# Performance work log

Measured on AMD Instinct MI355X. Metric: run time of the kernel, lower is better.

Reference implementation:

```python
import jax, jax.numpy as jnp
import numpy as np

N = 50000   # nodes
E = 800000  # edges (avg degree 16)
D = 128     # input feature dim
H = 128     # hidden dim
C = 10      # num classes
G = 16      # graphs in batch


def setup_inputs() -> dict:
    key = jax.random.key(0)
    ks = jax.random.split(key, 12)
    def w(k, shape):
        return jax.random.normal(k, shape, jnp.float32) / np.sqrt(shape[0]).astype(np.float32)
    return {
        "h": jax.random.normal(ks[0], (N, D), jnp.float32),
        "src": jax.random.randint(ks[1], (E,), 0, N, jnp.int32),
        "dst": jax.random.randint(ks[2], (E,), 0, N, jnp.int32),
        "graph_ids": jnp.sort(jax.random.randint(ks[3], (N,), 0, G, jnp.int32)),
        "W1a": w(ks[4], (D, H)), "b1a": jnp.zeros((H,), jnp.float32),
        "W2a": w(ks[5], (H, H)), "b2a": jnp.zeros((H,), jnp.float32),
        "W1b": w(ks[6], (H, H)), "b1b": jnp.zeros((H,), jnp.float32),
        "W2b": w(ks[7], (H, H)), "b2b": jnp.zeros((H,), jnp.float32),
        "Wc1": w(ks[8], (H, H)), "bc1": jnp.zeros((H,), jnp.float32),
        "Wc2": w(ks[9], (H, C)), "bc2": jnp.zeros((C,), jnp.float32),
    }


def _gin_layer(h, src, dst, W1, b1, W2, b2):
    # GIN aggregation, eps=0: z_i = h_i + sum_{j in N(i)} h_j
    agg = jax.ops.segment_sum(h[src], dst, num_segments=N)
    z = h + agg
    # 2-layer MLP apply function with relu activation ('relu' arg of GINLayer)
    z = jax.nn.relu(z @ W1 + b1)
    return jax.nn.relu(z @ W2 + b2)


def reference(h, src, dst, graph_ids, W1a, b1a, W2a, b2a,
              W1b, b1b, W2b, b2b, Wc1, bc1, Wc2, bc2):
    h = _gin_layer(h, src, dst, W1a, b1a, W2a, b2a)   # [N, H]
    h = _gin_layer(h, src, dst, W1b, b1b, W2b, b2b)   # [N, H]
    # dgl.mean_nodes over the batched graph
    sums = jax.ops.segment_sum(h, graph_ids, num_segments=G)                # [G, H]
    cnts = jax.ops.segment_sum(jnp.ones((N, 1), h.dtype), graph_ids, num_segments=G)
    h_g = sums / jnp.maximum(cnts, 1.0)
    # cls MLP: linear -> relu -> linear (logits)
    out = jax.nn.relu(h_g @ Wc1 + bc1) @ Wc2 + bc2    # [G, C]
    return out
```

## Files before the change

kernel.cpp:

```cpp
#include <hip/hip_runtime.h>
#include <stdint.h>

#define NN 50000
#define EE 800000
#define DD 128
#define GG 16
#define CC 10
#define NBK 196
#define BCH 4096
#define SMAX 5120
#define FT (NBK * NBK)
#define NSCN ((FT + 255) / 256)
#define NT 782

typedef unsigned short u16;
typedef __bf16 bf16x8 __attribute__((ext_vector_type(8)));
typedef float f32x4 __attribute__((ext_vector_type(4)));
typedef unsigned int u32x4 __attribute__((ext_vector_type(4)));
typedef float fl4 __attribute__((ext_vector_type(4)));

__device__ inline u16 f2bf(float f) {
    unsigned u = __float_as_uint(f);
    u = u + 0x7fffu + ((u >> 16) & 1u);
    return (u16)(u >> 16);
}
__device__ inline unsigned pack2(float a, float b) {
    return (unsigned)f2bf(a) | ((unsigned)f2bf(b) << 16);
}
__device__ inline float bf2f(unsigned bits16) { return __uint_as_float(bits16 << 16); }
__device__ inline void acc8(float* a, uint4 v) {
    a[0] += __uint_as_float(v.x << 16); a[1] += __uint_as_float(v.x & 0xffff0000u);
    a[2] += __uint_as_float(v.y << 16); a[3] += __uint_as_float(v.y & 0xffff0000u);
    a[4] += __uint_as_float(v.z << 16); a[5] += __uint_as_float(v.z & 0xffff0000u);
    a[6] += __uint_as_float(v.w << 16); a[7] += __uint_as_float(v.w & 0xffff0000u);
}
__device__ inline void mand(uint4& v, int p) {
    unsigned m = p ? 0xffffffffu : 0u;
    v.x &= m; v.y &= m; v.z &= m; v.w &= m;
}
__device__ inline void nt_store16(void* p, uint4 v) {
    u32x4 x; x.x = v.x; x.y = v.y; x.z = v.z; x.w = v.w;
    __builtin_nontemporal_store(x, (u32x4*)p);
}
__device__ inline float4 nt_loadf4(const float* p) {
    fl4 x = __builtin_nontemporal_load((const fl4*)p);
    float4 r; r.x = x.x; r.y = x.y; r.z = x.z; r.w = x.w;
    return r;
}

#define PZ (GG * DD)
#define PC (NN * DD / 4)
#define PW (4 * DD * DD)
#define PTOT (PZ + PC + PW)
#define PBLK ((PTOT + 255) / 256)

__global__ __launch_bounds__(256) void prepsort_kernel(
    const float* __restrict__ h,
    const float* __restrict__ a, const float* __restrict__ b,
    const float* __restrict__ c, const float* __restrict__ d,
    int* __restrict__ zbase, u16* __restrict__ H0, u16* __restrict__ wt,
    const int* __restrict__ dst, int* __restrict__ counts) {
    __shared__ int hist[NBK];
    int blk = blockIdx.x, t = threadIdx.x;
    if (blk < NBK) {
        for (int i = t; i < NBK; i += 256) hist[i] = 0;
        __syncthreads();
        int e0 = blk * BCH, e1 = min(e0 + BCH, EE);
        for (int e = e0 + t; e < e1; e += 256) atomicAdd(&hist[dst[e] >> 8], 1);
        __syncthreads();
        for (int i = t; i < NBK; i += 256) counts[i * NBK + blk] = hist[i];
        return;
    }
    int i = (blk - NBK) * 256 + t;
    if (i < PZ) { zbase[i] = 0; return; }
    i -= PZ;
    if (i < PC) {
        int j = i * 4;
        float4 v = nt_loadf4(h + j);
        ushort4 o;
        o.x = f2bf(v.x); o.y = f2bf(v.y); o.z = f2bf(v.z); o.w = f2bf(v.w);
        *(ushort4*)(H0 + j) = o;
        return;
    }
    i -= PC;
    if (i < PW) {
        int m = i >> 14, r = i & 16383, k = r >> 7, j = r & 127;
        const float* W = (m == 0) ? a : (m == 1) ? b : (m == 2) ? c : d;
        wt[(m << 14) + (j << 7) + k] = f2bf(W[(k << 7) + j]);
    }
}

__global__ __launch_bounds__(256) void scanA_kernel(int* __restrict__ counts,
                                                    int* __restrict__ bsum) {
    __shared__ int tmp[256];
    int t = threadIdx.x, idx = blockIdx.x * 256 + t;
    int v = (idx < FT) ? counts[idx] : 0;
    tmp[t] = v; __syncthreads();
    for (int off = 1; off < 256; off <<= 1) {
        int x = (t >= off) ? tmp[t - off] : 0;
        __syncthreads();
        tmp[t] += x;
        __syncthreads();
    }
    if (idx < FT) counts[idx] = tmp[t] - v;
    if (t == 255) bsum[blockIdx.x] = tmp[255];
}

__global__ __launch_bounds__(256) void scanB_kernel(int* __restrict__ bsum,
                                                    const int* __restrict__ gids,
                                                    int* __restrict__ gstart) {
    __shared__ int tmp[256];
    int t = threadIdx.x;
    if (t <= GG) {
        int lo = 0, hi = NN;
        while (lo < hi) { int mid = (lo + hi) >> 1; if (gids[mid] < t) lo = mid + 1; else hi = mid; }
        gstart[t] = lo;
    }
    int v = (t < NSCN) ? bsum[t] : 0;
    tmp[t] = v; __syncthreads();
    for (int off = 1; off < 256; off <<= 1) {
        int x = (t >= off) ? tmp[t - off] : 0;
        __syncthreads();
        tmp[t] += x;
        __syncthreads();
    }
    if (t < NSCN) bsum[t] = tmp[t] - v;
}

__global__ __launch_bounds__(256) void scanC_kernel(int* __restrict__ counts,
                                                    const int* __restrict__ bsum) {
    int idx = blockIdx.x * 256 + threadIdx.x;
    if (idx < FT) counts[idx] += bsum[blockIdx.x];
}

__global__ __launch_bounds__(256) void sortP3_kernel(const int* __restrict__ src,
                                                     const int* __restrict__ dst,
                                                     const int* __restrict__ counts,
                                                     int* __restrict__ epack) {
    __shared__ int lhist[NBK + 1];
    __shared__ int lcur[NBK];
    __shared__ int goff[NBK];
    __shared__ int tmp[256];
    __shared__ int sbuf[BCH];
    int b = blockIdx.x, t = threadIdx.x;
    int e0 = b * BCH, e1 = min(e0 + BCH, EE), n = e1 - e0;

    for (int i = t; i < NBK; i += 256) lhist[i] = 0;
    __syncthreads();
    for (int e = e0 + t; e < e1; e += 256) atomicAdd(&lhist[dst[e] >> 8], 1);
    __syncthreads();
    int v = (t < NBK) ? lhist[t] : 0;
    tmp[t] = v; __syncthreads();
    for (int off = 1; off < 256; off <<= 1) {
        int x = (t >= off) ? tmp[t - off] : 0;
        __syncthreads();
        tmp[t] += x;
        __syncthreads();
    }
    if (t < NBK) {
        int excl = tmp[t] - v;
        lcur[t] = excl;
        lhist[t] = excl;
        goff[t] = counts[t * NBK + b] - excl;
    }
    if (t == 0) lhist[NBK] = n;
    __syncthreads();
    for (int e = e0 + t; e < e1; e += 256) {
        int dd = dst[e], s = src[e];
        int p = atomicAdd(&lcur[dd >> 8], 1);
        sbuf[p] = (s << 8) | (dd & 255);
    }
    __syncthreads();
    for (int i = t; i < n; i += 256) {
        int pk = sbuf[i];
        int lo = 0, hi = NBK - 1;
        while (lo < hi) { int mid = (lo + hi + 1) >> 1; if (lhist[mid] <= i) lo = mid; else hi = mid - 1; }
        epack[goff[lo] + i] = pk;
    }
}

__global__ __launch_bounds__(256) void sortP4_kernel(const int* __restrict__ epack,
                                                     const int* __restrict__ counts,
                                                     int* __restrict__ offs,
                                                     int* __restrict__ ssrc) {
    __shared__ int hist[256];
    __shared__ int curs[256];
    __shared__ int stage[SMAX];
    int j = blockIdx.x, t = threadIdx.x;
    int n0 = j << 8;
    int b0 = counts[j * NBK];
    int b1 = (j < NBK - 1) ? counts[(j + 1) * NBK] : EE;
    hist[t] = 0;
    __syncthreads();
    for (int e = b0 + t; e < b1; e += 256) atomicAdd(&hist[epack[e] & 255], 1);
    __syncthreads();
    int deg = hist[t];
    for (int off = 1; off < 256; off <<= 1) {
        int x = (t >= off) ? hist[t - off] : 0;
        __syncthreads();
        hist[t] += x;
        __syncthreads();
    }
    int loff = hist[t] - deg;
    curs[t] = loff;
    if (n0 + t <= NN) offs[n0 + t] = b0 + loff;
    __syncthreads();
    for (int e = b0 + t; e < b1; e += 256) {
        int pk = epack[e];
        int p = atomicAdd(&curs[pk & 255], 1);
        stage[p] = pk >> 8;
    }
    __syncthreads();
    int n = b1 - b0;
    for (int i = t; i < n; i += 256) ssrc[b0 + i] = stage[i];
}

__global__ __launch_bounds__(256) void agg_kernel(
    const u16* __restrict__ Hin, const int* __restrict__ offs,
    const int* __restrict__ ssrc, u16* __restrict__ Z) {
    int node = blockIdx.x * 16 + (threadIdx.x >> 4);
    int lid = threadIdx.x & 15;
    if (node >= NN) return;
    int foff = lid * 8;
    const u16* base = Hin + foff;

    float acc[8] = {0.f, 0.f, 0.f, 0.f, 0.f, 0.f, 0.f, 0.f};
    uint4 vs = *(const uint4*)(base + (size_t)node * DD);
    int e0 = offs[node], e1 = offs[node + 1];
    acc8(acc, vs);

    int nch = (e1 - e0 + 7) >> 3;
    if (nch > 0) {
        int elast = e1 - 1;
        int i0 = ssrc[e0];
        int i1 = ssrc[min(e0 + 1, elast)];
        int i2 = ssrc[min(e0 + 2, elast)];
        int i3 = ssrc[min(e0 + 3, elast)];
        int i4 = ssrc[min(e0 + 4, elast)];
        int i5 = ssrc[min(e0 + 5, elast)];
        int i6 = ssrc[min(e0 + 6, elast)];
        int i7 = ssrc[min(e0 + 7, elast)];
        int eb = e0;
        for (int c = 0; c < nch; c++) {
            int ebn = eb + 8;
            int n0 = i0, n1 = i1, n2 = i2, n3 = i3, n4 = i4, n5 = i5, n6 = i6, n7 = i7;
            if (c + 1 < nch) {
                n0 = ssrc[ebn];
                n1 = ssrc[min(ebn + 1, elast)];
                n2 = ssrc[min(ebn + 2, elast)];
                n3 = ssrc[min(ebn + 3, elast)];
                n4 = ssrc[min(ebn + 4, elast)];
                n5 = ssrc[min(ebn + 5, elast)];
                n6 = ssrc[min(ebn + 6, elast)];
                n7 = ssrc[min(ebn + 7, elast)];
            }
            uint4 v0 = *(const uint4*)(base + (size_t)i0 * DD);
            uint4 v1 = *(const uint4*)(base + (size_t)i1 * DD);
            uint4 v2 = *(const uint4*)(base + (size_t)i2 * DD);
            uint4 v3 = *(const uint4*)(base + (size_t)i3 * DD);
            uint4 v4 = *(const uint4*)(base + (size_t)i4 * DD);
            uint4 v5 = *(const uint4*)(base + (size_t)i5 * DD);
            uint4 v6 = *(const uint4*)(base + (size_t)i6 * DD);
            uint4 v7 = *(const uint4*)(base + (size_t)i7 * DD);
            mand(v1, eb + 1 < e1); mand(v2, eb + 2 < e1); mand(v3, eb + 3 < e1);
            mand(v4, eb + 4 < e1); mand(v5, eb + 5 < e1); mand(v6, eb + 6 < e1);
            mand(v7, eb + 7 < e1);
            acc8(acc, v0); acc8(acc, v1); acc8(acc, v2); acc8(acc, v3);
            acc8(acc, v4); acc8(acc, v5); acc8(acc, v6); acc8(acc, v7);
            i0 = n0; i1 = n1; i2 = n2; i3 = n3; i4 = n4; i5 = n5; i6 = n6; i7 = n7;
            eb = ebn;
        }
    }
    uint4 o;
    o.x = pack2(acc[0], acc[1]); o.y = pack2(acc[2], acc[3]);
    o.z = pack2(acc[4], acc[5]); o.w = pack2(acc[6], acc[7]);
    nt_store16(Z + (size_t)node * DD + foff, o);
}

__global__ __launch_bounds__(256, 1) void mlp_kernel(
    const u16* __restrict__ Zin, const u16* __restrict__ Wt1, const float* __restrict__ b1,
    const u16* __restrict__ Wt2, const float* __restrict__ b2,
    u16* __restrict__ Hout, const int* __restrict__ gids, float* __restrict__ pool) {
    __shared__ __align__(16) u16 w1f[16384];
    __shared__ __align__(16) u16 yb[64][136];
    const int tid = threadIdx.x;
    const int wave = tid >> 6;
    const int lane = tid & 63;
    const int m16 = lane & 15;
    const int quad = lane >> 4;

    for (int cidx = tid; cidx < 2048; cidx += 256) {
        int ln = cidx & 63, nt = (cidx >> 6) & 7, kk = cidx >> 9;
        int gofs = ((nt * 16 + (ln & 15)) << 7) + kk * 32 + (ln >> 4) * 8;
        *(uint4*)&w1f[cidx * 8] = *(const uint4*)(Wt1 + gofs);
    }
    bf16x8 w2r[4][8];
#pragma unroll
    for (int kk = 0; kk < 4; kk++)
#pragma unroll
        for (int nt = 0; nt < 8; nt++)
            w2r[kk][nt] = *(const bf16x8*)(Wt2 + ((nt * 16 + m16) << 7) + kk * 32 + quad * 8);
    float bias1[8], bias2[8];
#pragma unroll
    for (int nt = 0; nt < 8; nt++) {
        bias1[nt] = b1[nt * 16 + m16];
        bias2[nt] = b2[nt * 16 + m16];
    }
    __syncthreads();

    int tile = blockIdx.x;
    bf16x8 afr[4], afrN[4];
    {
        size_t row = (size_t)(tile * 64 + wave * 16 + m16);
#pragma unroll
        for (int kk = 0; kk < 4; kk++)
            afr[kk] = *(const bf16x8*)(Zin + row * DD + kk * 32 + quad * 8);
    }
    for (; tile < NT; tile += 256) {
        int nxt = tile + 256;
        if (nxt < NT) {
            size_t row = (size_t)(nxt * 64 + wave * 16 + m16);
#pragma unroll
            for (int kk = 0; kk < 4; kk++)
                afrN[kk] = *(const bf16x8*)(Zin + row * DD + kk * 32 + quad * 8);
        }
        const int row0 = tile * 64 + wave * 16;

        f32x4 acc[8];
#pragma unroll
        for (int nt = 0; nt < 8; nt++) acc[nt] = (f32x4){0.f, 0.f, 0.f, 0.f};
#pragma unroll
        for (int kk = 0; kk < 4; kk++) {
#pragma unroll
            for (int nt = 0; nt < 8; nt++) {
                bf16x8 bfr = *(const bf16x8*)&w1f[(((kk * 8 + nt) * 64) + lane) * 8];
                acc[nt] = __builtin_amdgcn_mfma_f32_16x16x32_bf16(afr[kk], bfr, acc[nt], 0, 0, 0);
            }
        }
#pragma unroll
        for (int nt = 0; nt < 8; nt++) {
            int col = nt * 16 + m16;
#pragma unroll
            for (int r = 0; r < 4; r++) {
                float yv = acc[nt][r] + bias1[nt];
                yv = yv > 0.f ? yv : 0.f;
                yb[wave * 16 + quad * 4 + r][col] = f2bf(yv);
            }
        }

        bf16x8 afr2[4];
#pragma unroll
        for (int kk = 0; kk < 4; kk++)
            afr2[kk] = *(const bf16x8*)&yb[wave * 16 + m16][kk * 32 + quad * 8];
#pragma unroll
        for (int nt = 0; nt < 8; nt++) acc[nt] = (f32x4){0.f, 0.f, 0.f, 0.f};
#pragma unroll
        for (int kk = 0; kk < 4; kk++) {
#pragma unroll
            for (int nt = 0; nt < 8; nt++)
                acc[nt] = __builtin_amdgcn_mfma_f32_16x16x32_bf16(afr2[kk], w2r[kk][nt], acc[nt], 0, 0, 0);
        }
#pragma unroll
        for (int nt = 0; nt < 8; nt++) {
            int col = nt * 16 + m16;
#pragma unroll
            for (int r = 0; r < 4; r++) {
                float ov = acc[nt][r] + bias2[nt];
                ov = ov > 0.f ? ov : 0.f;
                yb[wave * 16 + quad * 4 + r][col] = f2bf(ov);
            }
        }
        if (!pool) {
#pragma unroll
            for (int p = 0; p < 4; p++) {
                int idx = p * 64 + lane;
                int r = idx >> 4, ch = idx & 15;
                int grow = row0 + r;
                if (grow < NN)
                    *(uint4*)(Hout + (size_t)grow * DD + ch * 8) = *(const uint4*)&yb[wave * 16 + r][ch * 8];
            }
        } else {
            int prow = row0 + m16;
            int g = gids[min(prow, NN - 1)];
#pragma unroll
            for (int fsel = 0; fsel < 2; fsel++) {
                int f = lane + fsel * 64;
                float s = 0.f;
                int cur = __shfl(g, 0);
                for (int r = 0; r < 16; r++) {
                    int gr = __shfl(g, r);
                    float v = (row0 + r < NN) ? bf2f((unsigned)yb[wave * 16 + r][f]) : 0.f;
                    if (gr != cur) { atomicAdd(&pool[cur * DD + f], s); s = 0.f; cur = gr; }
                    s += v;
                }
                atomicAdd(&pool[cur * DD + f], s);
            }
        }
#pragma unroll
        for (int kk = 0; kk < 4; kk++) afr[kk] = afrN[kk];
    }
}

__global__ void cls_kernel(const float* __restrict__ pool, const int* __restrict__ gstart,
                           const float* __restrict__ Wc1, const float* __restrict__ bc1,
                           const float* __restrict__ Wc2, const float* __restrict__ bc2,
                           float* __restrict__ out) {
    __shared__ float hg[128];
    __shared__ float y1[128];
    int g = blockIdx.x;
    int t = threadIdx.x;
    int cnt = gstart[g + 1] - gstart[g];
    float inv = 1.f / (float)(cnt > 1 ? cnt : 1);
    hg[t] = pool[g * DD + t] * inv;
    __syncthreads();
    float a = bc1[t];
    for (int k = 0; k < DD; k++) a += hg[k] * Wc1[k * DD + t];
    y1[t] = a > 0.f ? a : 0.f;
    __syncthreads();
    if (t < CC) {
        float o = bc2[t];
        for (int k = 0; k < DD; k++) o += y1[k] * Wc2[k * CC + t];
        out[g * CC + t] = o;
    }
}

extern "C" void kernel_launch(void* const* d_in, const int* in_sizes, int n_in,
                              void* d_out, int out_size, void* d_ws, size_t ws_size,
                              hipStream_t stream) {
    const float* h    = (const float*)d_in[0];
    const int*   src  = (const int*)d_in[1];
    const int*   dst  = (const int*)d_in[2];
    const int*   gids = (const int*)d_in[3];
    const float* W1a  = (const float*)d_in[4];
    const float* b1a  = (const float*)d_in[5];
    const float* W2a  = (const float*)d_in[6];
    const float* b2a  = (const float*)d_in[7];
    const float* W1b  = (const float*)d_in[8];
    const float* b1b  = (const float*)d_in[9];
    const float* W2b  = (const float*)d_in[10];
    const float* b2b  = (const float*)d_in[11];
    const float* Wc1  = (const float*)d_in[12];
    const float* bc1  = (const float*)d_in[13];
    const float* Wc2  = (const float*)d_in[14];
    const float* bc2  = (const float*)d_in[15];
    float* out = (float*)d_out;

    char* ws = (char*)d_ws;
    u16*   H0     = (u16*)(ws);
    u16*   H1     = (u16*)(ws + 12800000);
    u16*   H2     = (u16*)(ws + 25600000);
    u16*   Wt     = (u16*)(ws + 38400000);
    float* pool   = (float*)(ws + 38531072);
    int*   offs   = (int*)(ws + 38539264);
    int*   ssrc   = (int*)(ws + 38739268);
    int*   gstart = (int*)(ws + 41939268);
    int*   counts = (int*)(ws + 41939336);
    int*   bsum   = (int*)(ws + 42093000);
    int*   epack  = (int*)(ws + 42093792);
    u16*   Z1     = H2;
    u16*   Z2     = H0;

    prepsort_kernel<<<dim3(NBK + PBLK), dim3(256), 0, stream>>>(
        h, W1a, W2a, W1b, W2b, (int*)pool, H0, Wt, dst, counts);
    scanA_kernel<<<dim3(NSCN), dim3(256), 0, stream>>>(counts, bsum);
    scanB_kernel<<<dim3(1), dim3(256), 0, stream>>>(bsum, gids, gstart);
    scanC_kernel<<<dim3(NSCN), dim3(256), 0, stream>>>(counts, bsum);
    sortP3_kernel<<<dim3(NBK), dim3(256), 0, stream>>>(src, dst, counts, epack);
    sortP4_kernel<<<dim3(NBK), dim3(256), 0, stream>>>(epack, counts, offs, ssrc);
    agg_kernel<<<dim3((NN + 15) / 16), dim3(256), 0, stream>>>(H0, offs, ssrc, Z1);
    mlp_kernel<<<dim3(256), dim3(256), 0, stream>>>(Z1, Wt, b1a, Wt + 16384, b2a, H1, gids, nullptr);
    agg_kernel<<<dim3((NN + 15) / 16), dim3(256), 0, stream>>>(H1, offs, ssrc, Z2);
    mlp_kernel<<<dim3(256), dim3(256), 0, stream>>>(Z2, Wt + 32768, b1b, Wt + 49152, b2b, H2, gids, pool);
    cls_kernel<<<dim3(GG), dim3(128), 0, stream>>>(pool, gstart, Wc1, bc1, Wc2, bc2, out);
}
```

Measured before the change: 250.9 us.

## Fuse scan stages and classifier into last-block-done tails of preceding kernels

Merges the three scan kernels into one using a last-block-finishes atomic counter. The second-level offsets are applied lazily in sortP3/sortP4 via bsum lookups instead of a separate scanC pass. The classifier kernel is folded into the tail of the second mlp kernel, run by whichever block finishes last, and the done counters are zeroed by the prep kernel. This removes three kernel launches and their dependency gaps, at the cost of threadfence/atomic synchronisation and a serial tail on a single block.

Result: slower. 294.4 us (+17.3%).

```diff
diff --git a/kernel.cpp b/kernel.cpp
--- a/kernel.cpp
+++ b/kernel.cpp
@@ -48,7 +48,7 @@
     return r;
 }
 
-#define PZ (GG * DD)
+#define PZ (GG * DD + 16)
 #define PC (NN * DD / 4)
 #define PW (4 * DD * DD)
 #define PTOT (PZ + PC + PW)
@@ -90,9 +90,13 @@
     }
 }
 
-__global__ __launch_bounds__(256) void scanA_kernel(int* __restrict__ counts,
-                                                    int* __restrict__ bsum) {
+__global__ __launch_bounds__(256) void scanAB_kernel(int* __restrict__ counts,
+                                                     int* __restrict__ bsum,
+                                                     int* __restrict__ done,
+                                                     const int* __restrict__ gids,
+                                                     int* __restrict__ gstart) {
     __shared__ int tmp[256];
+    __shared__ int amLast;
     int t = threadIdx.x, idx = blockIdx.x * 256 + t;
     int v = (idx < FT) ? counts[idx] : 0;
     tmp[t] = v; __syncthreads();
@@ -103,39 +107,32 @@
         __syncthreads();
     }
     if (idx < FT) counts[idx] = tmp[t] - v;
-    if (t == 255) bsum[blockIdx.x] = tmp[255];
-}
-
-__global__ __launch_bounds__(256) void scanB_kernel(int* __restrict__ bsum,
-                                                    const int* __restrict__ gids,
-                                                    int* __restrict__ gstart) {
-    __shared__ int tmp[256];
-    int t = threadIdx.x;
+    if (t == 255) atomicExch(&bsum[blockIdx.x], tmp[255]);
+    __threadfence();
+    __syncthreads();
+    if (t == 0) amLast = (atomicAdd(&done[0], 1) == NSCN - 1);
+    __syncthreads();
+    if (!amLast) return;
     if (t <= GG) {
         int lo = 0, hi = NN;
         while (lo < hi) { int mid = (lo + hi) >> 1; if (gids[mid] < t) lo = mid + 1; else hi = mid; }
         gstart[t] = lo;
     }
-    int v = (t < NSCN) ? bsum[t] : 0;
-    tmp[t] = v; __syncthreads();
+    int bv = (t < NSCN) ? atomicAdd(&bsum[t], 0) : 0;
+    tmp[t] = bv; __syncthreads();
     for (int off = 1; off < 256; off <<= 1) {
         int x = (t >= off) ? tmp[t - off] : 0;
         __syncthreads();
         tmp[t] += x;
         __syncthreads();
     }
-    if (t < NSCN) bsum[t] = tmp[t] - v;
-}
-
-__global__ __launch_bounds__(256) void scanC_kernel(int* __restrict__ counts,
-                                                    const int* __restrict__ bsum) {
-    int idx = blockIdx.x * 256 + threadIdx.x;
-    if (idx < FT) counts[idx] += bsum[blockIdx.x];
+    if (t < NSCN) bsum[t] = tmp[t] - bv;
 }
 
 __global__ __launch_bounds__(256) void sortP3_kernel(const int* __restrict__ src,
                                                      const int* __restrict__ dst,
                                                      const int* __restrict__ counts,
+                                                     const int* __restrict__ bsum,
                                                      int* __restrict__ epack) {
     __shared__ int lhist[NBK + 1];
     __shared__ int lcur[NBK];
@@ -161,7 +158,8 @@
         int excl = tmp[t] - v;
         lcur[t] = excl;
         lhist[t] = excl;
-        goff[t] = counts[t * NBK + b] - excl;
+        int fi = t * NBK + b;
+        goff[t] = counts[fi] + bsum[fi >> 8] - excl;
     }
     if (t == 0) lhist[NBK] = n;
     __syncthreads();
@@ -181,6 +179,7 @@
 
 __global__ __launch_bounds__(256) void sortP4_kernel(const int* __restrict__ epack,
                                                      const int* __restrict__ counts,
+                                                     const int* __restrict__ bsum,
                                                      int* __restrict__ offs,
                                                      int* __restrict__ ssrc) {
     __shared__ int hist[256];
@@ -188,8 +187,11 @@
     __shared__ int stage[SMAX];
     int j = blockIdx.x, t = threadIdx.x;
     int n0 = j << 8;
-    int b0 = counts[j * NBK];
-    int b1 = (j < NBK - 1) ? counts[(j + 1) * NBK] : EE;
+    int fi0 = j * NBK;
+    int b0 = counts[fi0] + bsum[fi0 >> 8];
+    int b1;
+    if (j < NBK - 1) { int fi1 = (j + 1) * NBK; b1 = counts[fi1] + bsum[fi1 >> 8]; }
+    else b1 = EE;
     hist[t] = 0;
     __syncthreads();
     for (int e = b0 + t; e < b1; e += 256) atomicAdd(&hist[epack[e] & 255], 1);
@@ -280,9 +282,14 @@
 __global__ __launch_bounds__(256, 1) void mlp_kernel(
     const u16* __restrict__ Zin, const u16* __restrict__ Wt1, const float* __restrict__ b1,
     const u16* __restrict__ Wt2, const float* __restrict__ b2,
-    u16* __restrict__ Hout, const int* __restrict__ gids, float* __restrict__ pool) {
+    u16* __restrict__ Hout, const int* __restrict__ gids, float* __restrict__ pool,
+    int* __restrict__ done2, const int* __restrict__ gstart,
+    const float* __restrict__ Wc1, const float* __restrict__ bc1,
+    const float* __restrict__ Wc2, const float* __restrict__ bc2,
+    float* __restrict__ out) {
     __shared__ __align__(16) u16 w1f[16384];
     __shared__ __align__(16) u16 yb[64][136];
+    __shared__ int amLast;
     const int tid = threadIdx.x;
     const int wave = tid >> 6;
     const int lane = tid & 63;
@@ -399,28 +406,33 @@
 #pragma unroll
         for (int kk = 0; kk < 4; kk++) afr[kk] = afrN[kk];
     }
-}
-
-__global__ void cls_kernel(const float* __restrict__ pool, const int* __restrict__ gstart,
-                           const float* __restrict__ Wc1, const float* __restrict__ bc1,
-                           const float* __restrict__ Wc2, const float* __restrict__ bc2,
-                           float* __restrict__ out) {
-    __shared__ float hg[128];
-    __shared__ float y1[128];
-    int g = blockIdx.x;
-    int t = threadIdx.x;
-    int cnt = gstart[g + 1] - gstart[g];
-    float inv = 1.f / (float)(cnt > 1 ? cnt : 1);
-    hg[t] = pool[g * DD + t] * inv;
-    __syncthreads();
-    float a = bc1[t];
-    for (int k = 0; k < DD; k++) a += hg[k] * Wc1[k * DD + t];
-    y1[t] = a > 0.f ? a : 0.f;
-    __syncthreads();
-    if (t < CC) {
-        float o = bc2[t];
-        for (int k = 0; k < DD; k++) o += y1[k] * Wc2[k * CC + t];
-        out[g * CC + t] = o;
+
+    if (pool) {
+        __threadfence();
+        if (tid == 0) amLast = (atomicAdd(done2, 1) == 255);
+        __syncthreads();
+        if (amLast) {
+            __shared__ float hg[2][128];
+            __shared__ float y1[2][128];
+            int half = tid >> 7, f = tid & 127;
+            for (int gp = 0; gp < GG; gp += 2) {
+                int g = gp + half;
+                int cnt = gstart[g + 1] - gstart[g];
+                float inv = 1.f / (float)(cnt > 1 ? cnt : 1);
+                hg[half][f] = atomicAdd(&pool[g * DD + f], 0.f) * inv;
+                __syncthreads();
+                float a2 = bc1[f];
+                for (int k = 0; k < DD; k++) a2 += hg[half][k] * Wc1[k * DD + f];
+                y1[half][f] = a2 > 0.f ? a2 : 0.f;
+                __syncthreads();
+                if (f < CC) {
+                    float o = bc2[f];
+                    for (int k = 0; k < DD; k++) o += y1[half][k] * Wc2[k * CC + f];
+                    out[g * CC + f] = o;
+                }
+                __syncthreads();
+            }
+        }
     }
 }
 
@@ -451,25 +463,27 @@
     u16*   H2     = (u16*)(ws + 25600000);
     u16*   Wt     = (u16*)(ws + 38400000);
     float* pool   = (float*)(ws + 38531072);
-    int*   offs   = (int*)(ws + 38539264);
-    int*   ssrc   = (int*)(ws + 38739268);
-    int*   gstart = (int*)(ws + 41939268);
-    int*   counts = (int*)(ws + 41939336);
-    int*   bsum   = (int*)(ws + 42093000);
-    int*   epack  = (int*)(ws + 42093792);
+    int*   done   = (int*)(ws + 38539264);
+    int*   offs   = (int*)(ws + 38539328);
+    int*   ssrc   = (int*)(ws + 38739332);
+    int*   gstart = (int*)(ws + 41939332);
+    int*   counts = (int*)(ws + 41939400);
+    int*   bsum   = (int*)(ws + 42093064);
+    int*   epack  = (int*)(ws + 42093696);
     u16*   Z1     = H2;
     u16*   Z2     = H0;
 
     prepsort_kernel<<<dim3(NBK + PBLK), dim3(256), 0, stream>>>(
         h, W1a, W2a, W1b, W2b, (int*)pool, H0, Wt, dst, counts);
-    scanA_kernel<<<dim3(NSCN), dim3(256), 0, stream>>>(counts, bsum);
-    scanB_kernel<<<dim3(1), dim3(256), 0, stream>>>(bsum, gids, gstart);
-    scanC_kernel<<<dim3(NSCN), dim3(256), 0, stream>>>(counts, bsum);
-    sortP3_kernel<<<dim3(NBK), dim3(256), 0, stream>>>(src, dst, counts, epack);
-    sortP4_kernel<<<dim3(NBK), dim3(256), 0, stream>>>(epack, counts, offs, ssrc);
+    scanAB_kernel<<<dim3(NSCN), dim3(256), 0, stream>>>(counts, bsum, done, gids, gstart);
+    sortP3_kernel<<<dim3(NBK), dim3(256), 0, stream>>>(src, dst, counts, bsum, epack);
+    sortP4_kernel<<<dim3(NBK), dim3(256), 0, stream>>>(epack, counts, bsum, offs, ssrc);
     agg_kernel<<<dim3((NN + 15) / 16), dim3(256), 0, stream>>>(H0, offs, ssrc, Z1);
-    mlp_kernel<<<dim3(256), dim3(256), 0, stream>>>(Z1, Wt, b1a, Wt + 16384, b2a, H1, gids, nullptr);
+    mlp_kernel<<<dim3(256), dim3(256), 0, stream>>>(Z1, Wt, b1a, Wt + 16384, b2a, H1,
+                                                    gids, nullptr, done + 1, gstart,
+                                                    Wc1, bc1, Wc2, bc2, out);
     agg_kernel<<<dim3((NN + 15) / 16), dim3(256), 0, stream>>>(H1, offs, ssrc, Z2);
-    mlp_kernel<<<dim3(256), dim3(256), 0, stream>>>(Z2, Wt + 32768, b1b, Wt + 49152, b2b, H2, gids, pool);
-    cls_kernel<<<dim3(GG), dim3(128), 0, stream>>>(pool, gstart, Wc1, bc1, Wc2, bc2, out);
-}
+    mlp_kernel<<<dim3(256), dim3(256), 0, stream>>>(Z2, Wt + 32768, b1b, Wt + 49152, b2b, H2,
+                                                    gids, pool, done + 1, gstart,
+                                                    Wc1, bc1, Wc2, bc2, out);
+}
```
